# Optimization experiments

Measured on AMD Instinct MI355X. Metric: run time of the kernel, lower is better.

The kernel has to match this reference:

```python
import jax, jax.numpy as jnp
import numpy as np

N_NODES = 50000
N_EDGES = 200000
IN_DIM = 512
HID = 2000
LAT = 128


def setup_inputs() -> dict:
    key = jax.random.key(0)
    ks = jax.random.split(key, 6)
    x = jax.random.normal(ks[0], (N_NODES, IN_DIM), dtype=jnp.float32)
    edge_index = jax.random.randint(ks[1], (2, N_EDGES), 0, N_NODES, dtype=jnp.int64)
    # glorot-ish scales so ReLU/Sigmoid stay in a sane range
    W1 = jax.random.normal(ks[2], (IN_DIM, HID), dtype=jnp.float32) * (1.0 / np.sqrt(IN_DIM))
    b1 = jnp.zeros((HID,), dtype=jnp.float32)
    W2 = jax.random.normal(ks[3], (HID, LAT), dtype=jnp.float32) * (1.0 / np.sqrt(HID))
    b2 = jnp.zeros((LAT,), dtype=jnp.float32)
    return {"x": x, "edge_index": edge_index, "W1": W1, "b1": b1, "W2": W2, "b2": b2}


def gcn_conv(x, edge_index, W, b):
    """PyG GCNConv: D^-1/2 (A+I) D^-1/2 (X W) + b, unit edge weights."""
    n = x.shape[0]
    loops = jnp.arange(n, dtype=edge_index.dtype)
    row = jnp.concatenate([edge_index[0], loops])  # source nodes
    col = jnp.concatenate([edge_index[1], loops])  # target nodes
    deg = jax.ops.segment_sum(jnp.ones_like(col, dtype=x.dtype), col, num_segments=n)
    dis = jnp.where(deg > 0, jax.lax.rsqrt(deg), 0.0)  # deg^-1/2, inf -> 0
    norm = dis[row] * dis[col]                         # [E+N]
    h = x @ W                                          # transform first: [N, out]
    msg = h[row] * norm[:, None]                       # gather + normalize: [E+N, out]
    out = jax.ops.segment_sum(msg, col, num_segments=n)  # scatter-add
    return out + b


def reference(x, edge_index, W1, b1, W2, b2):
    h = jax.nn.relu(gcn_conv(x, edge_index, W1, b1))
    return jax.nn.sigmoid(gcn_conv(h, edge_index, W2, b2))
```

## Files before the change

kernel.cpp:

```cpp
#include <hip/hip_runtime.h>
#include <hip/hip_fp16.h>

#define NN 50000
#define NE 200000
#define IND 512
#define HIDD 2000
#define LATD 128

#define M_PAD 50048
#define N1_PAD 2048

typedef _Float16 f16x8 __attribute__((ext_vector_type(8)));
typedef float f32x4 __attribute__((ext_vector_type(4)));

__device__ __forceinline__ void gload_lds16(const _Float16* g, _Float16* l) {
    __builtin_amdgcn_global_load_lds(
        (const __attribute__((address_space(1))) unsigned int*)g,
        (__attribute__((address_space(3))) unsigned int*)l,
        16, 0, 0);
}

__global__ void k_degree(const int* __restrict__ col, int* __restrict__ deg) {
    int e = blockIdx.x * 256 + threadIdx.x;
    if (e < NE) atomicAdd(&deg[col[e]], 1);
}

__global__ void k_dis(const int* __restrict__ deg, float* __restrict__ dis) {
    int i = blockIdx.x * 256 + threadIdx.x;
    if (i < NN) dis[i] = rsqrtf((float)deg[i] + 1.0f);
}

__global__ void k_scan(const int* __restrict__ deg, int* __restrict__ row_ptr) {
    __shared__ int smem[1024];
    const int tid = threadIdx.x;
    int carry = 0;
    for (int chunk = 0; chunk < NN; chunk += 1024) {
        int i = chunk + tid;
        int v = (i < NN) ? deg[i] : 0;
        smem[tid] = v;
        __syncthreads();
        #pragma unroll
        for (int off = 1; off < 1024; off <<= 1) {
            int t = (tid >= off) ? smem[tid - off] : 0;
            __syncthreads();
            if (tid >= off) smem[tid] += t;
            __syncthreads();
        }
        if (i < NN) row_ptr[i] = carry + smem[tid] - v;
        int tot = smem[1023];
        __syncthreads();
        carry += tot;
    }
    if (tid == 0) row_ptr[NN] = carry;
}

__global__ void k_fill(const int* __restrict__ ei, const int* __restrict__ row_ptr,
                       int* __restrict__ cursor, int* __restrict__ csr_src) {
    int e = blockIdx.x * 256 + threadIdx.x;
    if (e < NE) {
        int r = ei[e], c = ei[NE + e];
        int pos = atomicAdd(&cursor[c], 1);
        csr_src[row_ptr[c] + pos] = r;
    }
}

__global__ void k_transpose_cvt(const float* __restrict__ in,
                                _Float16* __restrict__ out, int R, int C, int ldo) {
    int idx = blockIdx.x * 256 + threadIdx.x;
    if (idx < R * C) {
        int r = idx / C, c = idx - r * C;
        out[c * ldo + r] = (_Float16)in[idx];
    }
}

__global__ void k_gather_x(const float* __restrict__ x, const int* __restrict__ row_ptr,
                           const int* __restrict__ csr_src, const float* __restrict__ dis,
                           _Float16* __restrict__ Ah) {
    int dst = blockIdx.x * 4 + (threadIdx.x >> 6);
    if (dst >= NN) return;
    int lane = threadIdx.x & 63;
    float dd = dis[dst];
    const float* xd = x + (size_t)dst * IND + lane * 8;
    float4 a0 = *(const float4*)xd;
    float4 a1 = *(const float4*)(xd + 4);
    float acc[8] = { dd*a0.x, dd*a0.y, dd*a0.z, dd*a0.w,
                     dd*a1.x, dd*a1.y, dd*a1.z, dd*a1.w };
    int beg = row_ptr[dst], end = row_ptr[dst + 1];
    for (int i = beg; i < end; ++i) {
        int s = csr_src[i];
        float ns = dis[s];
        const float* xs = x + (size_t)s * IND + lane * 8;
        float4 b0 = *(const float4*)xs;
        float4 b1 = *(const float4*)(xs + 4);
        acc[0] += ns * b0.x; acc[1] += ns * b0.y; acc[2] += ns * b0.z; acc[3] += ns * b0.w;
        acc[4] += ns * b1.x; acc[5] += ns * b1.y; acc[6] += ns * b1.z; acc[7] += ns * b1.w;
    }
    f16x8 o;
    #pragma unroll
    for (int i = 0; i < 8; ++i) o[i] = (_Float16)(dd * acc[i]);
    *(f16x8*)(Ah + (size_t)dst * IND + lane * 8) = o;
}

__global__ void k_gather_t(const float* __restrict__ t, const int* __restrict__ row_ptr,
                           const int* __restrict__ csr_src, const float* __restrict__ dis,
                           const float* __restrict__ b2, float* __restrict__ out) {
    int dst = blockIdx.x * 4 + (threadIdx.x >> 6);
    if (dst >= NN) return;
    int lane = threadIdx.x & 63;
    float dd = dis[dst];
    float2 td = *(const float2*)(t + (size_t)dst * LATD + lane * 2);
    float accx = dd * td.x, accy = dd * td.y;
    int beg = row_ptr[dst], end = row_ptr[dst + 1];
    for (int i = beg; i < end; ++i) {
        int s = csr_src[i];
        float ns = dis[s];
        float2 ts = *(const float2*)(t + (size_t)s * LATD + lane * 2);
        accx += ns * ts.x; accy += ns * ts.y;
    }
    float2 bb = *(const float2*)(b2 + lane * 2);
    float vx = dd * accx + bb.x;
    float vy = dd * accy + bb.y;
    float2 o;
    o.x = 1.0f / (1.0f + __expf(-vx));
    o.y = 1.0f / (1.0f + __expf(-vy));
    *(float2*)(out + (size_t)dst * LATD + lane * 2) = o;
}

template<bool RELU_BIAS>
__global__ __launch_bounds__(256, 2) void k_gemm_lds(
    const _Float16* __restrict__ A,
    const _Float16* __restrict__ Bt,
    const float* __restrict__ bias,
    _Float16* __restrict__ Ch,
    float* __restrict__ Cf,
    int N, int K)
{
    __shared__ __align__(16) _Float16 As[128 * 32];
    __shared__ __align__(16) _Float16 Bs[128 * 32];

    const int tid = threadIdx.x;
    const int lane = tid & 63;
    const int w = tid >> 6;
    const int mBase = blockIdx.x * 128;
    const int nBase = blockIdx.y * 128;

    const int srow = w * 32 + (lane >> 2);
    const int scol = (lane & 3) * 8;
    const _Float16* Ag0 = A + (size_t)(mBase + srow) * K + scol;
    const _Float16* Ag1 = Ag0 + (size_t)16 * K;
    const _Float16* Bg0 = Bt + (size_t)(nBase + srow) * K + scol;
    const _Float16* Bg1 = Bg0 + (size_t)16 * K;
    _Float16* Asl0 = As + w * 1024;
    _Float16* Asl1 = Asl0 + 512;
    _Float16* Bsl0 = Bs + w * 1024;
    _Float16* Bsl1 = Bsl0 + 512;

    const int wm = (w >> 1) * 64;
    const int wn = (w & 1) * 64;
    const int lm = lane & 15;
    const int quad = lane >> 4;

    f32x4 acc[4][4];
    #pragma unroll
    for (int i = 0; i < 4; ++i)
        #pragma unroll
        for (int j = 0; j < 4; ++j)
            acc[i][j] = (f32x4){0.f, 0.f, 0.f, 0.f};

    for (int k0 = 0; k0 < K; k0 += 32) {
        gload_lds16(Ag0 + k0, Asl0);
        gload_lds16(Ag1 + k0, Asl1);
        gload_lds16(Bg0 + k0, Bsl0);
        gload_lds16(Bg1 + k0, Bsl1);
        __syncthreads();

        f16x8 af[4], bfr[4];
        #pragma unroll
        for (int mi = 0; mi < 4; ++mi)
            af[mi] = *(const f16x8*)&As[(wm + mi * 16 + lm) * 32 + quad * 8];
        #pragma unroll
        for (int ni = 0; ni < 4; ++ni)
            bfr[ni] = *(const f16x8*)&Bs[(wn + ni * 16 + lm) * 32 + quad * 8];
        #pragma unroll
        for (int mi = 0; mi < 4; ++mi)
            #pragma unroll
            for (int ni = 0; ni < 4; ++ni)
                acc[mi][ni] = __builtin_amdgcn_mfma_f32_16x16x32_f16(
                    af[mi], bfr[ni], acc[mi][ni], 0, 0, 0);
        __syncthreads();
    }

    #pragma unroll
    for (int mi = 0; mi < 4; ++mi) {
        #pragma unroll
        for (int ni = 0; ni < 4; ++ni) {
            int col = nBase + wn + ni * 16 + lm;
            float bval = RELU_BIAS ? bias[col] : 0.f;
            #pragma unroll
            for (int r = 0; r < 4; ++r) {
                int rowg = mBase + wm + mi * 16 + quad * 4 + r;
                float v = acc[mi][ni][r];
                if (RELU_BIAS) {
                    v = fmaxf(v + bval, 0.f);
                    Ch[(size_t)rowg * N + col] = (_Float16)v;
                } else {
                    Cf[(size_t)rowg * N + col] = v;
                }
            }
        }
    }
}

extern "C" void kernel_launch(void* const* d_in, const int* in_sizes, int n_in,
                              void* d_out, int out_size, void* d_ws, size_t ws_size,
                              hipStream_t stream) {
    const float* x  = (const float*)d_in[0];
    const int* ei   = (const int*)d_in[1];
    const float* W1 = (const float*)d_in[2];
    const float* b1 = (const float*)d_in[3];
    const float* W2 = (const float*)d_in[4];
    const float* b2 = (const float*)d_in[5];
    float* out = (float*)d_out;

    char* p = (char*)d_ws;
    auto alloc = [&](size_t bytes) {
        char* q = p; p += (bytes + 255) & ~(size_t)255; return q;
    };
    int* deg        = (int*)alloc((size_t)NN * 4);
    int* row_ptr    = (int*)alloc((size_t)(NN + 1) * 4);
    int* cursor     = (int*)alloc((size_t)NN * 4);
    int* csr_src    = (int*)alloc((size_t)NE * 4);
    float* dis      = (float*)alloc((size_t)NN * 4);
    float* b1pad    = (float*)alloc((size_t)N1_PAD * 4);
    _Float16* W1T   = (_Float16*)alloc((size_t)N1_PAD * IND * 2);
    _Float16* W2T   = (_Float16*)alloc((size_t)LATD * N1_PAD * 2);
    _Float16* Ah    = (_Float16*)alloc((size_t)M_PAD * IND * 2);
    _Float16* h     = (_Float16*)alloc((size_t)M_PAD * N1_PAD * 2);
    float* t        = (float*)alloc((size_t)M_PAD * LATD * 4);

    hipMemsetAsync(deg,    0, (size_t)NN * 4, stream);
    hipMemsetAsync(cursor, 0, (size_t)NN * 4, stream);
    hipMemsetAsync(b1pad,  0, (size_t)N1_PAD * 4, stream);
    hipMemsetAsync(W1T,    0, (size_t)N1_PAD * IND * 2, stream);
    hipMemsetAsync(W2T,    0, (size_t)LATD * N1_PAD * 2, stream);
    hipMemcpyAsync(b1pad, b1, (size_t)HIDD * 4, hipMemcpyDeviceToDevice, stream);

    k_degree<<<(NE + 255) / 256, 256, 0, stream>>>(ei + NE, deg);
    k_dis<<<(NN + 255) / 256, 256, 0, stream>>>(deg, dis);
    k_scan<<<1, 1024, 0, stream>>>(deg, row_ptr);
    k_fill<<<(NE + 255) / 256, 256, 0, stream>>>(ei, row_ptr, cursor, csr_src);

    k_transpose_cvt<<<(IND * HIDD + 255) / 256, 256, 0, stream>>>(W1, W1T, IND, HIDD, IND);
    k_transpose_cvt<<<(HIDD * LATD + 255) / 256, 256, 0, stream>>>(W2, W2T, HIDD, LATD, N1_PAD);

    k_gather_x<<<(NN + 3) / 4, 256, 0, stream>>>(x, row_ptr, csr_src, dis, Ah);

    dim3 g1(M_PAD / 128, N1_PAD / 128);
    k_gemm_lds<true><<<g1, 256, 0, stream>>>(Ah, W1T, b1pad, h, nullptr, N1_PAD, IND);
    dim3 g2(M_PAD / 128, LATD / 128);
    k_gemm_lds<false><<<g2, 256, 0, stream>>>(h, W2T, nullptr, nullptr, t, LATD, N1_PAD);

    k_gather_t<<<(NN + 3) / 4, 256, 0, stream>>>(t, row_ptr, csr_src, dis, b2, out);
}
```

Measured before the change: 620.8 us.

## Tile weight transposes, swizzle GEMM1 blocks per XCD, shrink GEMM2 tiles

Replaces the element-wise weight transpose with an LDS-tiled transpose so both reads and writes are coalesced. GEMM1 now uses a 1D grid whose block index maps to M slabs grouped by b&7, presumably so each XCD works on a contiguous M slab and reuses A tiles in its L2. GEMM2 uses 64-row tiles instead of 128, doubling its block count to about 782 so the GPU is better filled for the long-K second GEMM. The tradeoff is some early-exit padding blocks in GEMM1 and lower per-block reuse in GEMM2.

```diff
diff --git a/kernel.cpp b/kernel.cpp
--- a/kernel.cpp
+++ b/kernel.cpp
@@ -9,6 +9,9 @@
 
 #define M_PAD 50048
 #define N1_PAD 2048
+#define MT1 391
+#define NT1 16
+#define SLAB1 49
 
 typedef _Float16 f16x8 __attribute__((ext_vector_type(8)));
 typedef float f32x4 __attribute__((ext_vector_type(4)));
@@ -64,12 +67,21 @@
     }
 }
 
-__global__ void k_transpose_cvt(const float* __restrict__ in,
-                                _Float16* __restrict__ out, int R, int C, int ldo) {
-    int idx = blockIdx.x * 256 + threadIdx.x;
-    if (idx < R * C) {
-        int r = idx / C, c = idx - r * C;
-        out[c * ldo + r] = (_Float16)in[idx];
+__global__ void k_transpose_tiled(const float* __restrict__ in,
+                                  _Float16* __restrict__ out, int R, int C, int ldo) {
+    __shared__ float sm[32][33];
+    int c0 = blockIdx.x * 32, r0 = blockIdx.y * 32;
+    int tx = threadIdx.x & 31, ty = threadIdx.x >> 5;
+    #pragma unroll
+    for (int i = 0; i < 4; ++i) {
+        int r = r0 + ty + i * 8, c = c0 + tx;
+        sm[ty + i * 8][tx] = (r < R && c < C) ? in[(size_t)r * C + c] : 0.f;
+    }
+    __syncthreads();
+    #pragma unroll
+    for (int i = 0; i < 4; ++i) {
+        int c = c0 + ty + i * 8, r = r0 + tx;
+        if (c < C && r < R) out[(size_t)c * ldo + r] = (_Float16)sm[tx][ty + i * 8];
     }
 }
 
@@ -126,30 +138,32 @@
     *(float2*)(out + (size_t)dst * LATD + lane * 2) = o;
 }
 
-template<bool RELU_BIAS>
-__global__ __launch_bounds__(256, 2) void k_gemm_lds(
+__global__ __launch_bounds__(256, 2) void k_gemm1(
     const _Float16* __restrict__ A,
     const _Float16* __restrict__ Bt,
     const float* __restrict__ bias,
-    _Float16* __restrict__ Ch,
-    float* __restrict__ Cf,
-    int N, int K)
+    _Float16* __restrict__ Ch)
 {
+    const int b = blockIdx.x;
+    const int mT = (b & 7) * SLAB1 + ((b >> 3) >> 4);
+    const int nT = (b >> 3) & 15;
+    if (mT >= MT1) return;
+    const int mBase = mT * 128;
+    const int nBase = nT * 128;
+
     __shared__ __align__(16) _Float16 As[128 * 32];
     __shared__ __align__(16) _Float16 Bs[128 * 32];
 
     const int tid = threadIdx.x;
     const int lane = tid & 63;
     const int w = tid >> 6;
-    const int mBase = blockIdx.x * 128;
-    const int nBase = blockIdx.y * 128;
 
     const int srow = w * 32 + (lane >> 2);
     const int scol = (lane & 3) * 8;
-    const _Float16* Ag0 = A + (size_t)(mBase + srow) * K + scol;
-    const _Float16* Ag1 = Ag0 + (size_t)16 * K;
-    const _Float16* Bg0 = Bt + (size_t)(nBase + srow) * K + scol;
-    const _Float16* Bg1 = Bg0 + (size_t)16 * K;
+    const _Float16* Ag0 = A + (size_t)(mBase + srow) * IND + scol;
+    const _Float16* Ag1 = Ag0 + (size_t)16 * IND;
+    const _Float16* Bg0 = Bt + (size_t)(nBase + srow) * IND + scol;
+    const _Float16* Bg1 = Bg0 + (size_t)16 * IND;
     _Float16* Asl0 = As + w * 1024;
     _Float16* Asl1 = Asl0 + 512;
     _Float16* Bsl0 = Bs + w * 1024;
@@ -167,7 +181,7 @@
         for (int j = 0; j < 4; ++j)
             acc[i][j] = (f32x4){0.f, 0.f, 0.f, 0.f};
 
-    for (int k0 = 0; k0 < K; k0 += 32) {
+    for (int k0 = 0; k0 < IND; k0 += 32) {
         gload_lds16(Ag0 + k0, Asl0);
         gload_lds16(Ag1 + k0, Asl1);
         gload_lds16(Bg0 + k0, Bsl0);
@@ -195,17 +209,83 @@
         #pragma unroll
         for (int ni = 0; ni < 4; ++ni) {
             int col = nBase + wn + ni * 16 + lm;
-            float bval = RELU_BIAS ? bias[col] : 0.f;
+            float bval = bias[col];
             #pragma unroll
             for (int r = 0; r < 4; ++r) {
                 int rowg = mBase + wm + mi * 16 + quad * 4 + r;
-                float v = acc[mi][ni][r];
-                if (RELU_BIAS) {
-                    v = fmaxf(v + bval, 0.f);
-                    Ch[(size_t)rowg * N + col] = (_Float16)v;
-                } else {
-                    Cf[(size_t)rowg * N + col] = v;
-                }
+                float v = fmaxf(acc[mi][ni][r] + bval, 0.f);
+                Ch[(size_t)rowg * N1_PAD + col] = (_Float16)v;
+            }
+        }
+    }
+}
+
+__global__ __launch_bounds__(256, 2) void k_gemm2(
+    const _Float16* __restrict__ A,
+    const _Float16* __restrict__ Bt,
+    float* __restrict__ Cf)
+{
+    __shared__ __align__(16) _Float16 As[64 * 32];
+    __shared__ __align__(16) _Float16 Bs[128 * 32];
+
+    const int tid = threadIdx.x;
+    const int lane = tid & 63;
+    const int w = tid >> 6;
+    const int mBase = blockIdx.x * 64;
+
+    const int srA = w * 16 + (lane >> 2);
+    const int srB = w * 32 + (lane >> 2);
+    const int scol = (lane & 3) * 8;
+    const _Float16* Ag  = A + (size_t)(mBase + srA) * N1_PAD + scol;
+    const _Float16* Bg0 = Bt + (size_t)srB * N1_PAD + scol;
+    const _Float16* Bg1 = Bg0 + (size_t)16 * N1_PAD;
+    _Float16* Asl  = As + w * 512;
+    _Float16* Bsl0 = Bs + w * 1024;
+    _Float16* Bsl1 = Bsl0 + 512;
+
+    const int wm = (w & 1) * 32;
+    const int wn = (w >> 1) * 64;
+    const int lm = lane & 15;
+    const int quad = lane >> 4;
+
+    f32x4 acc[2][4];
+    #pragma unroll
+    for (int i = 0; i < 2; ++i)
+        #pragma unroll
+        for (int j = 0; j < 4; ++j)
+            acc[i][j] = (f32x4){0.f, 0.f, 0.f, 0.f};
+
+    for (int k0 = 0; k0 < N1_PAD; k0 += 32) {
+        gload_lds16(Ag + k0, Asl);
+        gload_lds16(Bg0 + k0, Bsl0);
+        gload_lds16(Bg1 + k0, Bsl1);
+        __syncthreads();
+
+        f16x8 af[2], bfr[4];
+        #pragma unroll
+        for (int mi = 0; mi < 2; ++mi)
+            af[mi] = *(const f16x8*)&As[(wm + mi * 16 + lm) * 32 + quad * 8];
+        #pragma unroll
+        for (int ni = 0; ni < 4; ++ni)
+            bfr[ni] = *(const f16x8*)&Bs[(wn + ni * 16 + lm) * 32 + quad * 8];
+        #pragma unroll
+        for (int mi = 0; mi < 2; ++mi)
+            #pragma unroll
+            for (int ni = 0; ni < 4; ++ni)
+                acc[mi][ni] = __builtin_amdgcn_mfma_f32_16x16x32_f16(
+                    af[mi], bfr[ni], acc[mi][ni], 0, 0, 0);
+        __syncthreads();
+    }
+
+    #pragma unroll
+    for (int mi = 0; mi < 2; ++mi) {
+        #pragma unroll
+        for (int ni = 0; ni < 4; ++ni) {
+            int col = wn + ni * 16 + lm;
+            #pragma unroll
+            for (int r = 0; r < 4; ++r) {
+                int rowg = mBase + wm + mi * 16 + quad * 4 + r;
+                Cf[(size_t)rowg * LATD + col] = acc[mi][ni][r];
             }
         }
     }
@@ -250,15 +330,17 @@
     k_scan<<<1, 1024, 0, stream>>>(deg, row_ptr);
     k_fill<<<(NE + 255) / 256, 256, 0, stream>>>(ei, row_ptr, cursor, csr_src);
 
-    k_transpose_cvt<<<(IND * HIDD + 255) / 256, 256, 0, stream>>>(W1, W1T, IND, HIDD, IND);
-    k_transpose_cvt<<<(HIDD * LATD + 255) / 256, 256, 0, stream>>>(W2, W2T, HIDD, LATD, N1_PAD);
+    {
+        dim3 gt1((HIDD + 31) / 32, (IND + 31) / 32);
+        k_transpose_tiled<<<gt1, 256, 0, stream>>>(W1, W1T, IND, HIDD, IND);
+        dim3 gt2((LATD + 31) / 32, (HIDD + 31) / 32);
+        k_transpose_tiled<<<gt2, 256, 0, stream>>>(W2, W2T, HIDD, LATD, N1_PAD);
+    }
 
     k_gather_x<<<(NN + 3) / 4, 256, 0, stream>>>(x, row_ptr, csr_src, dis, Ah);
 
-    dim3 g1(M_PAD / 128, N1_PAD / 128);
-    k_gemm_lds<true><<<g1, 256, 0, stream>>>(Ah, W1T, b1pad, h, nullptr, N1_PAD, IND);
-    dim3 g2(M_PAD / 128, LATD / 128);
-    k_gemm_lds<false><<<g2, 256, 0, stream>>>(h, W2T, nullptr, nullptr, t, LATD, N1_PAD);
+    k_gemm1<<<8 * SLAB1 * NT1, 256, 0, stream>>>(Ah, W1T, b1pad, h);
+    k_gemm2<<<M_PAD / 64, 256, 0, stream>>>(h, W2T, t);
 
     k_gather_t<<<(NN + 3) / 4, 256, 0, stream>>>(t, row_ptr, csr_src, dis, b2, out);
 }
```

Result: faster. 597.1 us (-3.8%).
